# Kernel optimization log

Measured on AMD Instinct MI355X. Metric: run time of the kernel, lower is better.

## Reference

```python
import jax, jax.numpy as jnp
import numpy as np

N_NODES = 100000
N_EDGES = 3200000
DIMS = [9, 18, 54, 108]


def setup_inputs() -> dict:
    key = jax.random.key(0)
    ks = jax.random.split(key, 10)
    inp = {
        "x": jax.random.normal(ks[0], (N_NODES, DIMS[0]), dtype=jnp.float32),
        "edge_index": jax.random.randint(ks[1], (2, N_EDGES), 0, N_NODES, dtype=jnp.int64),
        "edge_weight": jax.random.uniform(ks[2], (N_EDGES,), dtype=jnp.float32),
    }
    # Glorot-ish init for GCN weights, zero bias (PyG default bias init is zeros)
    for i in range(3):
        fan_in, fan_out = DIMS[i], DIMS[i + 1]
        s = (6.0 / (fan_in + fan_out)) ** 0.5
        inp[f"W{i+1}"] = jax.random.uniform(ks[3 + i], (fan_in, fan_out), jnp.float32, -s, s)
        inp[f"b{i+1}"] = jnp.zeros((fan_out,), dtype=jnp.float32)
    return inp


def _gcn_norm(edge_index, edge_weight, n_nodes):
    # Add self loops with weight 1, then symmetric normalization (PyG gcn_norm).
    loop = jnp.arange(n_nodes, dtype=edge_index.dtype)
    src = jnp.concatenate([edge_index[0], loop])
    dst = jnp.concatenate([edge_index[1], loop])
    w = jnp.concatenate([edge_weight, jnp.ones((n_nodes,), edge_weight.dtype)])
    deg = jax.ops.segment_sum(w, dst, num_segments=n_nodes)  # [N]
    dis = jnp.where(deg > 0, jax.lax.rsqrt(jnp.where(deg > 0, deg, 1.0)), 0.0)
    norm = dis[src] * w * dis[dst]  # [E+N]
    return src, dst, norm


def _gcn_layer(x, W, b, src, dst, norm, n_nodes):
    h = x @ W                              # [N, out] small GEMM
    msg = h[src] * norm[:, None]           # gather + scale  [E+N, out]
    out = jax.ops.segment_sum(msg, dst, num_segments=n_nodes)  # scatter-add
    return out + b


def reference(x, edge_index, edge_weight, W1, b1, W2, b2, W3, b3):
    n = x.shape[0]
    src, dst, norm = _gcn_norm(edge_index, edge_weight, n)
    h = jax.nn.relu(_gcn_layer(x, W1, b1, src, dst, norm, n))
    h = jax.nn.relu(_gcn_layer(h, W2, b2, src, dst, norm, n))
    h = jax.nn.relu(_gcn_layer(h, W3, b3, src, dst, norm, n))
    return h
```

## Files before the change

### kernel.cpp

```cpp
#include <hip/hip_runtime.h>
#include <hip/hip_fp16.h>

#define NN 100000
#define NE 3200000
#define NB 391
#define BCAP 9216

static inline int cdiv(long long a, int b) { return (int)((a + b - 1) / b); }

__global__ __launch_bounds__(1024) void k_scatterB(
    const int4* __restrict__ dst4, const int4* __restrict__ src4,
    const float4* __restrict__ w4, int* __restrict__ bsize, int2* __restrict__ barr) {
    __shared__ int hcnt[NB];
    __shared__ int hbase[NB];
    int t = threadIdx.x;
    if (t < NB) hcnt[t] = 0;
    __syncthreads();
    int idx = blockIdx.x * 1024 + t;
    bool valid = idx < (NE / 4);
    int4 d4 = valid ? dst4[idx] : make_int4(-1, -1, -1, -1);
    int dd[4] = {d4.x, d4.y, d4.z, d4.w};
    int rk[4];
#pragma unroll
    for (int k = 0; k < 4; ++k)
        if (dd[k] >= 0) rk[k] = atomicAdd(&hcnt[dd[k] >> 8], 1);
    __syncthreads();
    if (t < NB) {
        int c = hcnt[t];
        hbase[t] = (c > 0) ? atomicAdd(&bsize[t], c) : 0;
    }
    __syncthreads();
    if (!valid) return;
    int4 s4 = src4[idx];
    float4 wv = w4[idx];
    int ss[4] = {s4.x, s4.y, s4.z, s4.w};
    float ww[4] = {wv.x, wv.y, wv.z, wv.w};
#pragma unroll
    for (int k = 0; k < 4; ++k) {
        int d = dd[k];
        int bk = d >> 8;
        int pos = hbase[bk] + rk[k];
        if (pos < BCAP) {
            int key = ((d & 255) << 17) | ss[k];
            barr[(size_t)bk * BCAP + pos] = make_int2(key, __float_as_int(ww[k]));
        }
    }
}

__global__ void k_scanBB(const int* __restrict__ bsize, int* __restrict__ bbase) {
    __shared__ int s[512];
    int t = threadIdx.x;
    int v = (t < NB) ? bsize[t] : 0;
    s[t] = v;
    __syncthreads();
    for (int d = 1; d < 512; d <<= 1) {
        int a = (t >= d) ? s[t - d] : 0;
        __syncthreads();
        s[t] += a;
        __syncthreads();
    }
    if (t < NB) bbase[t] = s[t] - v;
}

__global__ __launch_bounds__(1024) void k_bucketCSR(
    const int2* __restrict__ barr, const int* __restrict__ bsize, const int* __restrict__ bbase,
    int* __restrict__ rowptr, float* __restrict__ dis, unsigned int* __restrict__ e2,
    const float* __restrict__ x, __half* __restrict__ y1) {
    __shared__ int cnt[256];
    __shared__ float wsum[256];
    __shared__ int rbase[256];
    __shared__ int sc[256];
    int b = blockIdx.x;
    int t = threadIdx.x;
    int nE = bsize[b];
    int ebase = bbase[b];
    const int2* rec = barr + (size_t)b * BCAP;
    if (t < 256) { cnt[t] = 0; wsum[t] = 0.0f; }
    __syncthreads();
    int rk[9];
#pragma unroll
    for (int k = 0; k < 9; ++k) {
        int e = t + (k << 10);
        if (e < nE) {
            int2 r = rec[e];
            int dl = (r.x >> 17) & 255;
            rk[k] = atomicAdd(&cnt[dl], 1);
            atomicAdd(&wsum[dl], __int_as_float(r.y));
        }
    }
    __syncthreads();
    int v = 0;
    if (t < 256) { v = cnt[t]; sc[t] = v; }
    __syncthreads();
    for (int d = 1; d < 256; d <<= 1) {
        int a = (t >= d && t < 256) ? sc[t - d] : 0;
        __syncthreads();
        if (t < 256) sc[t] += a;
        __syncthreads();
    }
    if (t < 256) {
        rbase[t] = sc[t] - v;
        int node = (b << 8) + t;
        float disv = rsqrtf(1.0f + wsum[t]);
        if (node < NN) {
            rowptr[node] = ebase + rbase[t];
            dis[node] = disv;
        }
        if (node == NN) rowptr[NN] = ebase + rbase[t];
        wsum[t] = disv;
    }
    __syncthreads();
#pragma unroll
    for (int k = 0; k < 9; ++k) {
        int e = t + (k << 10);
        if (e < nE) {
            int2 r = rec[e];
            int dl = (r.x >> 17) & 255;
            float wv = __int_as_float(r.y);
            int q = (int)(wv * 32768.0f + 0.5f);
            q = (q > 32767) ? 32767 : q;
            e2[(size_t)(ebase + rbase[dl] + rk[k])] =
                ((unsigned int)(r.x & 0x1FFFF) << 15) | (unsigned int)q;
        }
    }
    int nbase = b << 8;
#pragma unroll
    for (int k = 0; k < 3; ++k) {
        int idx = (k << 10) + t;
        if (idx < 2304) {
            int nl = idx / 9;
            int f = idx - nl * 9;
            int nd = nbase + nl;
            if (nd < NN)
                y1[(size_t)nd * 16 + f] = __float2half(x[(size_t)nd * 9 + f] * wsum[nl]);
        }
    }
}

template <int LPN, int YS, int OS>
__global__ void k_agg4(const __half* __restrict__ yin, const float* __restrict__ dis,
                       const int* __restrict__ rowptr, const unsigned int* __restrict__ e2,
                       float* __restrict__ agg, int n) {
    constexpr int NPW = 64 / LPN;
    int wv = threadIdx.x >> 6;
    int l = threadIdx.x & 63;
    int ni = l / LPN;
    int sub = l - ni * LPN;
    if (ni >= NPW) return;
    int i = (blockIdx.x * 4 + wv) * NPW + ni;
    if (i >= n) return;

    float acc0, acc1, acc2, acc3;
    {
        float2 raw = *(const float2*)(yin + (size_t)i * YS + sub * 4);
        __half2 ha = *(__half2*)&raw.x;
        __half2 hb = *(__half2*)&raw.y;
        acc0 = __low2float(ha); acc1 = __high2float(ha);
        acc2 = __low2float(hb); acc3 = __high2float(hb);
    }

    int e0 = rowptr[i];
    int e1 = rowptr[i + 1];
    int e = e0;
    const float QS = 1.0f / 32768.0f;
    for (; e + 8 <= e1; e += 8) {
        unsigned int r[8];
#pragma unroll
        for (int k = 0; k < 8; ++k) r[k] = e2[e + k];
        float2 raw[8];
#pragma unroll
        for (int k = 0; k < 8; ++k)
            raw[k] = *(const float2*)(yin + (size_t)(r[k] >> 15) * YS + sub * 4);
#pragma unroll
        for (int k = 0; k < 8; ++k) {
            float wq = (float)(r[k] & 32767u) * QS;
            __half2 ha = *(__half2*)&raw[k].x;
            __half2 hb = *(__half2*)&raw[k].y;
            acc0 = fmaf(__low2float(ha), wq, acc0);
            acc1 = fmaf(__high2float(ha), wq, acc1);
            acc2 = fmaf(__low2float(hb), wq, acc2);
            acc3 = fmaf(__high2float(hb), wq, acc3);
        }
    }
    for (; e < e1; ++e) {
        unsigned int r = e2[e];
        float wq = (float)(r & 32767u) * QS;
        float2 raw = *(const float2*)(yin + (size_t)(r >> 15) * YS + sub * 4);
        __half2 ha = *(__half2*)&raw.x;
        __half2 hb = *(__half2*)&raw.y;
        acc0 = fmaf(__low2float(ha), wq, acc0);
        acc1 = fmaf(__high2float(ha), wq, acc1);
        acc2 = fmaf(__low2float(hb), wq, acc2);
        acc3 = fmaf(__high2float(hb), wq, acc3);
    }

    float di = dis[i];
    float4* orow = (float4*)(agg + (size_t)i * OS + sub * 4);
    *orow = make_float4(acc0 * di, acc1 * di, acc2 * di, acc3 * di);
}

template <int FIN, int IS, int FOUT, int OSPLIT, int OS, bool SCALE, bool HALF_OUT>
__global__ __launch_bounds__(256) void k_gemm4(
    const float* __restrict__ agg, const float* __restrict__ W,
    const float* __restrict__ bias, const float* __restrict__ dis,
    void* __restrict__ outp, int n) {
    constexpr int CH = FOUT / OSPLIT;
    constexpr int NGRP = 4 / OSPLIT;
    int wv = threadIdx.x >> 6;
    int l = threadIdx.x & 63;
    int j = __builtin_amdgcn_readfirstlane(wv & (OSPLIT - 1));
    int grp = wv >> ((OSPLIT == 4) ? 2 : (OSPLIT == 2) ? 1 : 0);
    int i = (blockIdx.x * NGRP + grp) * 64 + l;
    if (i >= n) return;

    float row[FIN];
    const float* arow = agg + (size_t)i * IS;
#pragma unroll
    for (int f = 0; f < FIN; ++f) row[f] = arow[f];
    float sc = SCALE ? dis[i] : 1.0f;
    const float* Wj = W + j * CH;
    const float* bj = bias + j * CH;
    float acc[CH];
#pragma unroll
    for (int jj = 0; jj < CH; ++jj) acc[jj] = bj[jj];
#pragma unroll
    for (int f = 0; f < FIN; ++f) {
#pragma unroll
        for (int jj = 0; jj < CH; ++jj)
            acc[jj] = fmaf(row[f], Wj[f * FOUT + jj], acc[jj]);
    }
    if (HALF_OUT) {
        __half* orow = (__half*)outp + (size_t)i * OS + j * CH;
#pragma unroll
        for (int jj = 0; jj < CH; ++jj)
            orow[jj] = __float2half(fmaxf(acc[jj], 0.0f) * sc);
    } else {
        float* orow = (float*)outp + (size_t)i * OS + j * CH;
#pragma unroll
        for (int jj = 0; jj < CH; ++jj) orow[jj] = fmaxf(acc[jj], 0.0f) * sc;
    }
}

extern "C" void kernel_launch(void* const* d_in, const int* in_sizes, int n_in,
                              void* d_out, int out_size, void* d_ws, size_t ws_size,
                              hipStream_t stream) {
    const float* x  = (const float*)d_in[0];
    const int*   ei = (const int*)d_in[1];
    const float* ew = (const float*)d_in[2];
    const float* W1 = (const float*)d_in[3];
    const float* b1 = (const float*)d_in[4];
    const float* W2 = (const float*)d_in[5];
    const float* b2 = (const float*)d_in[6];
    const float* W3 = (const float*)d_in[7];
    const float* b3 = (const float*)d_in[8];
    float* out = (float*)d_out;

    const int* src = ei;
    const int* dst = ei + NE;

    char* ws = (char*)d_ws;
    size_t off = 0;
    auto alloc = [&](size_t bytes) {
        char* p = ws + off;
        off += (bytes + 511) / 512 * 512;
        return p;
    };
    float*        dis    = (float*)alloc((size_t)NN * 4);
    int*          rowptr = (int*)alloc((size_t)(NN + 1) * 4);
    int*          bsize  = (int*)alloc(NB * 4);
    int*          bbase  = (int*)alloc(NB * 4);
    unsigned int* e2     = (unsigned int*)alloc((size_t)NE * 4);
    float*        bufA   = (float*)alloc((size_t)NN * 56 * 4);
    __half*       y2     = (__half*)alloc((size_t)NN * 32 * 2);
    __half*       y3     = (__half*)alloc((size_t)NN * 64 * 2);
    __half*       y1     = (__half*)alloc((size_t)NN * 16 * 2);

    int2* barr = (int2*)bufA;

    const int B = 256;

    hipMemsetAsync(bsize, 0, NB * 4, stream);
    k_scatterB<<<cdiv(NE / 4, 1024), 1024, 0, stream>>>(
        (const int4*)dst, (const int4*)src, (const float4*)ew, bsize, barr);
    k_scanBB<<<1, 512, 0, stream>>>(bsize, bbase);
    k_bucketCSR<<<NB, 1024, 0, stream>>>(barr, bsize, bbase, rowptr, dis, e2, x, y1);

    const int NPB9  = (64 / 3) * 4;
    const int NPB18 = (64 / 5) * 4;
    const int NPB54 = (64 / 14) * 4;

    k_agg4<3, 16, 12><<<cdiv(NN, NPB9), B, 0, stream>>>(y1, dis, rowptr, e2, bufA, NN);
    k_gemm4<9, 12, 18, 2, 32, true, true><<<cdiv(NN, 128), B, 0, stream>>>(bufA, W1, b1, dis, y2, NN);

    k_agg4<5, 32, 20><<<cdiv(NN, NPB18), B, 0, stream>>>(y2, dis, rowptr, e2, bufA, NN);
    k_gemm4<18, 20, 54, 2, 64, true, true><<<cdiv(NN, 128), B, 0, stream>>>(bufA, W2, b2, dis, y3, NN);

    k_agg4<14, 64, 56><<<cdiv(NN, NPB54), B, 0, stream>>>(y3, dis, rowptr, e2, bufA, NN);
    k_gemm4<54, 56, 108, 4, 108, false, false><<<cdiv(NN, 64), B, 0, stream>>>(bufA, W3, b3, dis, out, NN);
}
```

Baseline: 273.1 us.

## Halve bucket size, fuse bucket scan into CSR build, store aggregates as fp16

Buckets now cover 128 destination nodes, which doubles the block count for the CSR build and shrinks per-block capacity. The separate bucket-offset scan kernel is removed and each CSR block redoes a 1024-wide prefix scan over bucket sizes itself. Aggregation outputs are written as fp16 instead of fp32, which halves intermediate traffic into the GEMM kernels at some precision cost. Workspace buffers are aliased onto the bucket array region to reduce footprint.

Result: faster. 266.9 us (-2.3%).

```diff
diff --git a/kernel.cpp b/kernel.cpp
--- a/kernel.cpp
+++ b/kernel.cpp
@@ -3,8 +3,8 @@
 
 #define NN 100000
 #define NE 3200000
-#define NB 391
-#define BCAP 9216
+#define NB 782
+#define BCAP 4864
 
 static inline int cdiv(long long a, int b) { return (int)((a + b - 1) / b); }
 
@@ -23,7 +23,7 @@
     int rk[4];
 #pragma unroll
     for (int k = 0; k < 4; ++k)
-        if (dd[k] >= 0) rk[k] = atomicAdd(&hcnt[dd[k] >> 8], 1);
+        if (dd[k] >= 0) rk[k] = atomicAdd(&hcnt[dd[k] >> 7], 1);
     __syncthreads();
     if (t < NB) {
         int c = hcnt[t];
@@ -38,69 +38,63 @@
 #pragma unroll
     for (int k = 0; k < 4; ++k) {
         int d = dd[k];
-        int bk = d >> 8;
+        int bk = d >> 7;
         int pos = hbase[bk] + rk[k];
         if (pos < BCAP) {
-            int key = ((d & 255) << 17) | ss[k];
+            int key = ((d & 127) << 17) | ss[k];
             barr[(size_t)bk * BCAP + pos] = make_int2(key, __float_as_int(ww[k]));
         }
     }
 }
 
-__global__ void k_scanBB(const int* __restrict__ bsize, int* __restrict__ bbase) {
-    __shared__ int s[512];
-    int t = threadIdx.x;
-    int v = (t < NB) ? bsize[t] : 0;
-    s[t] = v;
-    __syncthreads();
-    for (int d = 1; d < 512; d <<= 1) {
-        int a = (t >= d) ? s[t - d] : 0;
-        __syncthreads();
-        s[t] += a;
-        __syncthreads();
-    }
-    if (t < NB) bbase[t] = s[t] - v;
-}
-
 __global__ __launch_bounds__(1024) void k_bucketCSR(
-    const int2* __restrict__ barr, const int* __restrict__ bsize, const int* __restrict__ bbase,
+    const int2* __restrict__ barr, const int* __restrict__ bsize,
     int* __restrict__ rowptr, float* __restrict__ dis, unsigned int* __restrict__ e2,
     const float* __restrict__ x, __half* __restrict__ y1) {
-    __shared__ int cnt[256];
-    __shared__ float wsum[256];
-    __shared__ int rbase[256];
-    __shared__ int sc[256];
+    __shared__ int cnt[128];
+    __shared__ float wsum[128];
+    __shared__ int rbase[128];
+    __shared__ int sc[128];
+    __shared__ int sbs[1024];
     int b = blockIdx.x;
     int t = threadIdx.x;
     int nE = bsize[b];
-    int ebase = bbase[b];
+    nE = (nE < BCAP) ? nE : BCAP;
     const int2* rec = barr + (size_t)b * BCAP;
-    if (t < 256) { cnt[t] = 0; wsum[t] = 0.0f; }
-    __syncthreads();
-    int rk[9];
-#pragma unroll
-    for (int k = 0; k < 9; ++k) {
+    if (t < 128) { cnt[t] = 0; wsum[t] = 0.0f; }
+    sbs[t] = (t < NB) ? bsize[t] : 0;
+    __syncthreads();
+    for (int d = 1; d < 1024; d <<= 1) {
+        int a = (t >= d) ? sbs[t - d] : 0;
+        __syncthreads();
+        sbs[t] += a;
+        __syncthreads();
+    }
+    int ebase = (b > 0) ? sbs[b - 1] : 0;
+    int rk[5];
+#pragma unroll
+    for (int k = 0; k < 5; ++k) {
         int e = t + (k << 10);
         if (e < nE) {
             int2 r = rec[e];
-            int dl = (r.x >> 17) & 255;
+            int dl = (r.x >> 17) & 127;
             rk[k] = atomicAdd(&cnt[dl], 1);
             atomicAdd(&wsum[dl], __int_as_float(r.y));
         }
     }
     __syncthreads();
     int v = 0;
-    if (t < 256) { v = cnt[t]; sc[t] = v; }
-    __syncthreads();
-    for (int d = 1; d < 256; d <<= 1) {
-        int a = (t >= d && t < 256) ? sc[t - d] : 0;
+    if (t < 128) { v = cnt[t]; sc[t] = v; }
+    __syncthreads();
+    for (int d = 1; d < 128; d <<= 1) {
+        int a = (t >= d && t < 128) ? sc[t - d] : 0;
         __syncthreads();
-        if (t < 256) sc[t] += a;
+        if (t < 128) sc[t] += a;
         __syncthreads();
     }
-    if (t < 256) {
+    if (t < 128) {
         rbase[t] = sc[t] - v;
-        int node = (b << 8) + t;
+        int node = (b << 7) + t;
         float disv = rsqrtf(1.0f + wsum[t]);
         if (node < NN) {
             rowptr[node] = ebase + rbase[t];
@@ -111,11 +105,11 @@
     }
     __syncthreads();
 #pragma unroll
-    for (int k = 0; k < 9; ++k) {
+    for (int k = 0; k < 5; ++k) {
         int e = t + (k << 10);
         if (e < nE) {
             int2 r = rec[e];
-            int dl = (r.x >> 17) & 255;
+            int dl = (r.x >> 17) & 127;
             float wv = __int_as_float(r.y);
             int q = (int)(wv * 32768.0f + 0.5f);
             q = (q > 32767) ? 32767 : q;
@@ -123,11 +117,11 @@
                 ((unsigned int)(r.x & 0x1FFFF) << 15) | (unsigned int)q;
         }
     }
-    int nbase = b << 8;
-#pragma unroll
-    for (int k = 0; k < 3; ++k) {
+    int nbase = b << 7;
+#pragma unroll
+    for (int k = 0; k < 2; ++k) {
         int idx = (k << 10) + t;
-        if (idx < 2304) {
+        if (idx < 1152) {
             int nl = idx / 9;
             int f = idx - nl * 9;
             int nd = nbase + nl;
@@ -140,7 +134,7 @@
 template <int LPN, int YS, int OS>
 __global__ void k_agg4(const __half* __restrict__ yin, const float* __restrict__ dis,
                        const int* __restrict__ rowptr, const unsigned int* __restrict__ e2,
-                       float* __restrict__ agg, int n) {
+                       __half* __restrict__ agg, int n) {
     constexpr int NPW = 64 / LPN;
     int wv = threadIdx.x >> 6;
     int l = threadIdx.x & 63;
@@ -195,17 +189,22 @@
     }
 
     float di = dis[i];
-    float4* orow = (float4*)(agg + (size_t)i * OS + sub * 4);
-    *orow = make_float4(acc0 * di, acc1 * di, acc2 * di, acc3 * di);
+    __half2 o01 = __floats2half2_rn(acc0 * di, acc1 * di);
+    __half2 o23 = __floats2half2_rn(acc2 * di, acc3 * di);
+    float2 pk;
+    *(__half2*)&pk.x = o01;
+    *(__half2*)&pk.y = o23;
+    *(float2*)(agg + (size_t)i * OS + sub * 4) = pk;
 }
 
 template <int FIN, int IS, int FOUT, int OSPLIT, int OS, bool SCALE, bool HALF_OUT>
 __global__ __launch_bounds__(256) void k_gemm4(
-    const float* __restrict__ agg, const float* __restrict__ W,
+    const __half* __restrict__ agg, const float* __restrict__ W,
     const float* __restrict__ bias, const float* __restrict__ dis,
     void* __restrict__ outp, int n) {
     constexpr int CH = FOUT / OSPLIT;
     constexpr int NGRP = 4 / OSPLIT;
+    constexpr int NC = (FIN + 3) / 4;
     int wv = threadIdx.x >> 6;
     int l = threadIdx.x & 63;
     int j = __builtin_amdgcn_readfirstlane(wv & (OSPLIT - 1));
@@ -213,10 +212,18 @@
     int i = (blockIdx.x * NGRP + grp) * 64 + l;
     if (i >= n) return;
 
-    float row[FIN];
-    const float* arow = agg + (size_t)i * IS;
-#pragma unroll
-    for (int f = 0; f < FIN; ++f) row[f] = arow[f];
+    float row[NC * 4];
+    const float2* arow2 = (const float2*)(agg + (size_t)i * IS);
+#pragma unroll
+    for (int c = 0; c < NC; ++c) {
+        float2 raw = arow2[c];
+        __half2 ha = *(__half2*)&raw.x;
+        __half2 hb = *(__half2*)&raw.y;
+        row[c * 4 + 0] = __low2float(ha);
+        row[c * 4 + 1] = __high2float(ha);
+        row[c * 4 + 2] = __low2float(hb);
+        row[c * 4 + 3] = __high2float(hb);
+    }
     float sc = SCALE ? dis[i] : 1.0f;
     const float* Wj = W + j * CH;
     const float* bj = bias + j * CH;
@@ -268,22 +275,21 @@
     float*        dis    = (float*)alloc((size_t)NN * 4);
     int*          rowptr = (int*)alloc((size_t)(NN + 1) * 4);
     int*          bsize  = (int*)alloc(NB * 4);
-    int*          bbase  = (int*)alloc(NB * 4);
     unsigned int* e2     = (unsigned int*)alloc((size_t)NE * 4);
-    float*        bufA   = (float*)alloc((size_t)NN * 56 * 4);
-    __half*       y2     = (__half*)alloc((size_t)NN * 32 * 2);
-    __half*       y3     = (__half*)alloc((size_t)NN * 64 * 2);
+    char*         barrR  = alloc((size_t)NB * BCAP * 8);
     __half*       y1     = (__half*)alloc((size_t)NN * 16 * 2);
 
-    int2* barr = (int2*)bufA;
+    int2*   barr = (int2*)barrR;
+    __half* bufA = (__half*)barrR;
+    __half* y2   = (__half*)(barrR + 11200000);
+    __half* y3   = (__half*)(barrR + 17600000);
 
     const int B = 256;
 
     hipMemsetAsync(bsize, 0, NB * 4, stream);
     k_scatterB<<<cdiv(NE / 4, 1024), 1024, 0, stream>>>(
         (const int4*)dst, (const int4*)src, (const float4*)ew, bsize, barr);
-    k_scanBB<<<1, 512, 0, stream>>>(bsize, bbase);
-    k_bucketCSR<<<NB, 1024, 0, stream>>>(barr, bsize, bbase, rowptr, dis, e2, x, y1);
+    k_bucketCSR<<<NB, 1024, 0, stream>>>(barr, bsize, rowptr, dis, e2, x, y1);
 
     const int NPB9  = (64 / 3) * 4;
     const int NPB18 = (64 / 5) * 4;
```
